# Kernel optimization log

Hardware: AMD Instinct MI355X
Metric: run time of the kernel (lower is better)

Reference implementation:

```python
import jax, jax.numpy as jnp
import numpy as np
from jax import lax

T, B, I, H = 512, 32, 1024, 1024


def setup_inputs() -> dict:
    key = jax.random.key(0)
    ks = jax.random.split(key, 9)
    s = 1.0 / np.sqrt(H)
    u = lambda k, shape: jax.random.uniform(k, shape, jnp.float32, -s, s)
    return {
        "x": jax.random.normal(ks[0], (T, B, I), jnp.float32),
        "h0_fwd": jnp.zeros((B, H), jnp.float32),
        "c0_fwd": jnp.zeros((B, H), jnp.float32),
        "h0_bwd": jnp.zeros((B, H), jnp.float32),
        "c0_bwd": jnp.zeros((B, H), jnp.float32),
        "Wih_f": u(ks[1], (4 * H, I)), "Whh_f": u(ks[2], (4 * H, H)),
        "bih_f": u(ks[3], (4 * H,)), "bhh_f": u(ks[4], (4 * H,)),
        "Wih_b": u(ks[5], (4 * H, I)), "Whh_b": u(ks[6], (4 * H, H)),
        "bih_b": u(ks[7], (4 * H,)), "bhh_b": u(ks[8], (4 * H,)),
    }


def _lstm_dir(x, h0, c0, Wih, Whh, bih, bhh, reverse):
    # Precompute input-to-gate projections for all timesteps: [T, B, 4H]
    xg = jnp.einsum('tbi,gi->tbg', x, Wih) + bih + bhh
    WhhT = Whh.T  # [H, 4H]

    def step(carry, xg_t):
        h, c = carry
        gates = xg_t + h @ WhhT  # [B, 4H]
        i, f, g, o = jnp.split(gates, 4, axis=-1)
        i = jax.nn.sigmoid(i)
        f = jax.nn.sigmoid(f)
        g = jnp.tanh(g)
        o = jax.nn.sigmoid(o)
        c = f * c + i * g
        h = o * jnp.tanh(c)
        return (h, c), h

    (hT, cT), ys = lax.scan(step, (h0, c0), xg, reverse=reverse)
    return ys, hT, cT


def reference(x, h0_fwd, c0_fwd, h0_bwd, c0_bwd,
              Wih_f, Whh_f, bih_f, bhh_f,
              Wih_b, Whh_b, bih_b, bhh_b):
    out_f, hf, cf = _lstm_dir(x, h0_fwd, c0_fwd, Wih_f, Whh_f, bih_f, bhh_f, reverse=False)
    out_b, hb, cb = _lstm_dir(x, h0_bwd, c0_bwd, Wih_b, Whh_b, bih_b, bhh_b, reverse=True)
    out = jnp.concatenate([out_f, out_b], axis=-1)  # [T, B, 2H]
    return out, (hf, cf), (hb, cb)
```

## Files before the change

kernel.cpp:

```cpp
#include <hip/hip_runtime.h>
#include <stdint.h>


using short8 = __attribute__((ext_vector_type(8))) short;
using f32x4  = __attribute__((ext_vector_type(4))) float;
using f32x2  = __attribute__((ext_vector_type(2))) float;
using f32x16 = __attribute__((ext_vector_type(16))) float;
using h2f    = __attribute__((ext_vector_type(2))) _Float16;

typedef unsigned int uint;
typedef unsigned short ushort;
typedef unsigned long long ull;

typedef const __attribute__((address_space(1))) void cg_void;
typedef __attribute__((address_space(3))) void lds_void;

#define OFF_XB      0ull
#define OFF_WIH_F   33554432ull
#define OFF_WIH_B   41943040ull
#define OFF_WHH_F   50331648ull
#define OFF_WHH_B   58720256ull
#define OFF_BSUM_F  67108864ull
#define OFF_BSUM_B  67125248ull
#define OFF_HBUF    67141632ull
#define OFF_CBUF    67665920ull
#define OFF_XG      67928064ull


__device__ __forceinline__ ushort f2bf(float f) {
    uint u = __float_as_uint(f);
    u += 0x7fffu + ((u >> 16) & 1u);
    return (ushort)(u >> 16);
}
__device__ __forceinline__ float sigmoidf_(float x) { return 1.0f / (1.0f + expf(-x)); }

__global__ __launch_bounds__(256) void prep_kernel(
    const float* __restrict__ x,
    const float* __restrict__ wih_f, const float* __restrict__ whh_f,
    const float* __restrict__ bih_f, const float* __restrict__ bhh_f,
    const float* __restrict__ wih_b, const float* __restrict__ whh_b,
    const float* __restrict__ bih_b, const float* __restrict__ bhh_b,
    const float* __restrict__ h0f, const float* __restrict__ h0b,
    char* __restrict__ ws)
{
    int r = blockIdx.x * 256 + threadIdx.x;
    const int n_x = 16777216, n_w = 4194304;
    if (r < n_x) { ((ushort*)(ws + OFF_XB))[r] = f2bf(x[r]); return; }
    r -= n_x;
    if (r < n_w) { ((ushort*)(ws + OFF_WIH_F))[r] = f2bf(wih_f[r]); return; }
    r -= n_w;
    if (r < n_w) { ((ushort*)(ws + OFF_WIH_B))[r] = f2bf(wih_b[r]); return; }
    r -= n_w;
    if (r < n_w) { ((ushort*)(ws + OFF_WHH_F))[r] = f2bf(whh_f[r]); return; }
    r -= n_w;
    if (r < n_w) { ((ushort*)(ws + OFF_WHH_B))[r] = f2bf(whh_b[r]); return; }
    r -= n_w;
    if (r < 4096) { ((float*)(ws + OFF_BSUM_F))[r] = bih_f[r] + bhh_f[r]; return; }
    r -= 4096;
    if (r < 4096) { ((float*)(ws + OFF_BSUM_B))[r] = bih_b[r] + bhh_b[r]; return; }
    r -= 4096;
    if (r < 16384) {
        int b = r >> 9, wi = r & 511;
        uint pay = (uint)f2bf(h0f[b * 1024 + wi * 2]) |
                   ((uint)f2bf(h0f[b * 1024 + wi * 2 + 1]) << 16);
        ((ull*)(ws + OFF_HBUF))[r] = (ull)pay;
        return;
    }
    r -= 16384;
    if (r < 16384) {
        int b = r >> 9, wi = r & 511;
        uint pay = (uint)f2bf(h0b[b * 1024 + wi * 2]) |
                   ((uint)f2bf(h0b[b * 1024 + wi * 2 + 1]) << 16);
        ((ull*)(ws + OFF_HBUF))[2 * 16384 + r] = (ull)pay;
        return;
    }
    r -= 16384;
    if (r < 32768) {
        size_t wd = (r < 16384) ? (size_t)(16384 + r) : (size_t)(3 * 16384 + (r - 16384));
        ((ull*)(ws + OFF_HBUF))[wd] = 0xFFFFFFFF00000000ull;
        return;
    }
}

__global__ __launch_bounds__(256) void gemm_xg(
    const ushort* __restrict__ xb,
    const ushort* __restrict__ wihf, const ushort* __restrict__ wihb,
    _Float16* __restrict__ xgf, _Float16* __restrict__ xgb,
    int s0)
{
    __shared__ ushort As[128 * 32];
    __shared__ ushort Bs[128 * 32];
    const int dir = blockIdx.z;
    const ushort* __restrict__ W = dir ? wihb : wihf;
    _Float16* __restrict__ xg = dir ? xgb : xgf;
    const int mBlk = blockIdx.x, nBlk = blockIdx.y;
    const int tid = threadIdx.x;
    const int w = tid >> 6, l = tid & 63;
    const int q = l >> 4, ml = l & 15;

    f32x4 acc[4][4];
    const f32x4 zero = {0.f, 0.f, 0.f, 0.f};
#pragma unroll
    for (int i = 0; i < 4; ++i)
#pragma unroll
        for (int j = 0; j < 4; ++j) acc[i][j] = zero;

    for (int kb = 0; kb < 32; ++kb) {
#pragma unroll
        for (int it = 0; it < 2; ++it) {
            int idx = tid + 256 * it;
            int rl = idx >> 2, kc = idx & 3;
            int gr = mBlk * 128 + rl;
            int slot = gr >> 5, bb = gr & 31;
            int t = dir ? (511 - s0 - slot) : (s0 + slot);
            const ushort* ga = xb + (size_t)(t * 32 + bb) * 1024 + kb * 32 + kc * 8;
            __builtin_amdgcn_global_load_lds((cg_void*)ga, (lds_void*)(As + idx * 8), 16, 0, 0);
            int colg = nBlk * 128 + rl;
            const ushort* gbp = W + (size_t)colg * 1024 + kb * 32 + kc * 8;
            __builtin_amdgcn_global_load_lds((cg_void*)gbp, (lds_void*)(Bs + idx * 8), 16, 0, 0);
        }
        __syncthreads();
        short8 af[4], bfr[4];
#pragma unroll
        for (int i = 0; i < 4; ++i)
            af[i] = *(const short8*)(As + ((w & 1) * 64 + i * 16 + ml) * 32 + q * 8);
#pragma unroll
        for (int j = 0; j < 4; ++j)
            bfr[j] = *(const short8*)(Bs + ((w >> 1) * 64 + j * 16 + ml) * 32 + q * 8);
#pragma unroll
        for (int i = 0; i < 4; ++i)
#pragma unroll
            for (int j = 0; j < 4; ++j)
                acc[i][j] = __builtin_amdgcn_mfma_f32_16x16x32_bf16(af[i], bfr[j], acc[i][j], 0, 0, 0);
        __syncthreads();
    }
#pragma unroll
    for (int i = 0; i < 4; ++i)
#pragma unroll
        for (int j = 0; j < 4; ++j)
#pragma unroll
            for (int rr = 0; rr < 4; ++rr) {
                int row = mBlk * 128 + (w & 1) * 64 + i * 16 + q * 4 + rr;
                int col = nBlk * 128 + (w >> 1) * 64 + j * 16 + ml;
                xg[(size_t)row * 4096 + col] = (_Float16)acc[i][j][rr];
            }
}

__global__ __launch_bounds__(512, 1) void rec_kernel(
    const ushort* __restrict__ whhf, const ushort* __restrict__ whhb,
    const _Float16* __restrict__ xgf, const _Float16* __restrict__ xgb,
    const float* __restrict__ bsumf, const float* __restrict__ bsumb,
    const float* __restrict__ c0f, const float* __restrict__ c0b,
    ull* __restrict__ hbuf, float* __restrict__ cbuf,
    float* __restrict__ out,
    int s0, int csteps)
{
    __shared__ __align__(16) char lds_raw[65536];
    ushort* Hst = (ushort*)lds_raw;
    float*  gb  = (float*)lds_raw;

    const int bx = blockIdx.x;
    const int dir = bx & 1;
    const int p = bx >> 1;
    const int tid = threadIdx.x;
    const int w = tid >> 6;
    const int l = tid & 63;
    const int half = l >> 5;
    const int m32 = l & 31;
    const int nt = w & 3;
    const int kh = w >> 2;

    const ushort* W = dir ? whhb : whhf;
    const _Float16* xg = dir ? xgb : xgf;
    const float* bsum = dir ? bsumb : bsumf;

    const ushort* wrow = W + ((size_t)(nt * 1024 + p * 32 + m32)) * 1024 + kh * 512 + half * 8;
    short8 bfrag[32];
#pragma unroll
    for (int kk = 0; kk < 32; ++kk)
        bfrag[kk] = *(const short8*)(wrow + kk * 16);

    const int b = tid >> 4;
    const int rp = (tid & 15) * 2;
    const int hcol = p * 32 + rp;
    f32x2 bs[4];
#pragma unroll
    for (int g = 0; g < 4; ++g)
        bs[g] = *(const f32x2*)(bsum + g * 1024 + hcol);
    f32x2 cc;
    {
        const float* csrc = (s0 == 0) ? (dir ? c0b : c0f) : (cbuf + dir * 32768);
        cc = *(const f32x2*)(csrc + b * 1024 + hcol);
    }

    const int ch = tid >> 2;
    const int sub = (tid & 3) * 2;

    for (int s = s0; s < s0 + csteps; ++s) {
        const int slot = s - s0;
        const int t = dir ? (511 - s) : s;

        uint xv[4];
#pragma unroll
        for (int g = 0; g < 4; ++g)
            xv[g] = *(const uint*)(xg + ((size_t)slot * 32 + b) * 4096 + g * 1024 + hcol);

        const ull* hb64 = hbuf + (size_t)(dir * 2 + (s & 1)) * 16384;
        const uint su = (uint)s;
        {
            ull cur[8], nxt[8];
#pragma unroll
            for (int j = 0; j < 8; ++j)
                cur[j] = __hip_atomic_load(hb64 + j * 512 + tid,
                                           __ATOMIC_RELAXED, __HIP_MEMORY_SCOPE_AGENT);
#pragma unroll
            for (int gI = 0; gI < 4; ++gI) {
                if (gI < 3) {
#pragma unroll
                    for (int j = 0; j < 8; ++j)
                        nxt[j] = __hip_atomic_load(hb64 + (gI * 8 + 8 + j) * 512 + tid,
                                                   __ATOMIC_RELAXED, __HIP_MEMORY_SCOPE_AGENT);
                }
                for (;;) {
                    bool bad = false;
#pragma unroll
                    for (int j = 0; j < 8; ++j)
                        bad = bad || ((uint)(cur[j] >> 32) != su);
                    if (!__any(bad)) break;
#pragma unroll
                    for (int j = 0; j < 8; ++j)
                        if ((uint)(cur[j] >> 32) != su)
                            cur[j] = __hip_atomic_load(hb64 + (gI * 8 + j) * 512 + tid,
                                                       __ATOMIC_RELAXED, __HIP_MEMORY_SCOPE_AGENT);
                }
#pragma unroll
                for (int j = 0; j < 8; ++j) {
                    const int bb = gI * 8 + j;
                    *(uint*)(Hst + bb * 1024 + ((ch ^ (bb & 7)) << 3) + sub) = (uint)cur[j];
                }
                if (gI < 3) {
#pragma unroll
                    for (int j = 0; j < 8; ++j) cur[j] = nxt[j];
                }
            }
        }
        __syncthreads();

        f32x16 acce, acco;
#pragma unroll
        for (int i = 0; i < 16; ++i) { acce[i] = 0.f; acco[i] = 0.f; }
#pragma unroll
        for (int kk = 0; kk < 32; kk += 2) {
            const short8 a0 = *(const short8*)(Hst + m32 * 1024 +
                (((kh * 64 + kk * 2 + half) ^ (m32 & 7)) << 3));
            acce = __builtin_amdgcn_mfma_f32_32x32x16_bf16(a0, bfrag[kk], acce, 0, 0, 0);
            const short8 a1 = *(const short8*)(Hst + m32 * 1024 +
                (((kh * 64 + (kk + 1) * 2 + half) ^ (m32 & 7)) << 3));
            acco = __builtin_amdgcn_mfma_f32_32x32x16_bf16(a1, bfrag[kk + 1], acco, 0, 0, 0);
        }
        __syncthreads();

#pragma unroll
        for (int reg = 0; reg < 16; ++reg) {
            const int row = (reg & 3) + 8 * (reg >> 2) + 4 * half;
            gb[kh * 4128 + row * 129 + nt * 32 + m32] = acce[reg] + acco[reg];
        }
        __syncthreads();

        const float* gA = gb + b * 129 + rp;
        const float* gB = gb + 4128 + b * 129 + rp;
        f32x2 G[4];
#pragma unroll
        for (int g = 0; g < 4; ++g) {
            h2f xh = __builtin_bit_cast(h2f, xv[g]);
            G[g][0] = gA[g * 32]     + gB[g * 32]     + bs[g][0] + (float)xh[0];
            G[g][1] = gA[g * 32 + 1] + gB[g * 32 + 1] + bs[g][1] + (float)xh[1];
        }
        f32x2 hh;
#pragma unroll
        for (int j = 0; j < 2; ++j) {
            float ii = sigmoidf_(G[0][j]), ff2 = sigmoidf_(G[1][j]);
            float g2 = tanhf(G[2][j]),     oo  = sigmoidf_(G[3][j]);
            cc[j] = ff2 * cc[j] + ii * g2;
            hh[j] = oo * tanhf(cc[j]);
        }
        {
            uint pay = (uint)f2bf(hh[0]) | ((uint)f2bf(hh[1]) << 16);
            ull word = (ull)pay | ((ull)(uint)(s + 1) << 32);
            __hip_atomic_store(hbuf + (size_t)(dir * 2 + ((s + 1) & 1)) * 16384 +
                                   b * 512 + p * 16 + (tid & 15),
                               word, __ATOMIC_RELAXED, __HIP_MEMORY_SCOPE_AGENT);
        }

        __builtin_nontemporal_store(__builtin_bit_cast(double, hh),
            (double*)(out + (size_t)t * 65536 + b * 2048 + dir * 1024 + hcol));
        if (s == 511) {
            float* fin = out + 33554432 + dir * 65536;
            *(f32x2*)(fin + b * 1024 + hcol) = hh;
            *(f32x2*)(fin + 32768 + b * 1024 + hcol) = cc;
        }
        __syncthreads();
    }
    *(f32x2*)(cbuf + dir * 32768 + b * 1024 + hcol) = cc;
}

extern "C" void kernel_launch(void* const* d_in, const int* in_sizes, int n_in,
                              void* d_out, int out_size, void* d_ws, size_t ws_size,
                              hipStream_t stream)
{
    const float* x     = (const float*)d_in[0];
    const float* h0f   = (const float*)d_in[1];
    const float* c0f   = (const float*)d_in[2];
    const float* h0b   = (const float*)d_in[3];
    const float* c0b   = (const float*)d_in[4];
    const float* wih_f = (const float*)d_in[5];
    const float* whh_f = (const float*)d_in[6];
    const float* bih_f = (const float*)d_in[7];
    const float* bhh_f = (const float*)d_in[8];
    const float* wih_b = (const float*)d_in[9];
    const float* whh_b = (const float*)d_in[10];
    const float* bih_b = (const float*)d_in[11];
    const float* bhh_b = (const float*)d_in[12];
    float* out = (float*)d_out;
    char* ws = (char*)d_ws;

    int csteps = 16;
    const int cands[6] = {512, 256, 128, 64, 32, 16};
    for (int i = 0; i < 6; ++i) {
        size_t need = OFF_XG + 2ull * (size_t)cands[i] * 262144ull;
        if (need <= ws_size) { csteps = cands[i]; break; }
    }

    prep_kernel<<<131360, 256, 0, stream>>>(x, wih_f, whh_f, bih_f, bhh_f,
                                            wih_b, whh_b, bih_b, bhh_b, h0f, h0b, ws);

    const ushort* xb    = (const ushort*)(ws + OFF_XB);
    const ushort* wihfb = (const ushort*)(ws + OFF_WIH_F);
    const ushort* wihbb = (const ushort*)(ws + OFF_WIH_B);
    const ushort* whhfb = (const ushort*)(ws + OFF_WHH_F);
    const ushort* whhbb = (const ushort*)(ws + OFF_WHH_B);
    const float*  bsf   = (const float*)(ws + OFF_BSUM_F);
    const float*  bsb   = (const float*)(ws + OFF_BSUM_B);
    ull*    hb          = (ull*)(ws + OFF_HBUF);
    float*  cb          = (float*)(ws + OFF_CBUF);
    _Float16* xgfp      = (_Float16*)(ws + OFF_XG);
    _Float16* xgbp      = (_Float16*)(ws + OFF_XG + (size_t)csteps * 262144ull);

    const int nchunks = 512 / csteps;
    for (int cidx = 0; cidx < nchunks; ++cidx) {
        int s0 = cidx * csteps;
        gemm_xg<<<dim3(csteps / 4, 32, 2), 256, 0, stream>>>(xb, wihfb, wihbb, xgfp, xgbp, s0);

        const ushort* a0 = whhfb; const ushort* a1 = whhbb;
        const _Float16* a2 = xgfp; const _Float16* a3 = xgbp;
        const float* a4 = bsf; const float* a5 = bsb;
        const float* a6 = c0f; const float* a7 = c0b;
        ull* a8 = hb; float* a9 = cb; float* a10 = out;
        int a11 = s0, a12 = csteps;
        void* args[] = {&a0, &a1, &a2, &a3, &a4, &a5, &a6, &a7, &a8, &a9, &a10, &a11, &a12};
        hipLaunchCooperativeKernel((void*)rec_kernel, dim3(64), dim3(512), args, 0, stream);
    }
}
```

Baseline: 3.598 ms.

## Fuse input-projection GEMM with recurrence using producer blocks and per-slab counters

Replaces the chunked sequence of GEMM plus cooperative recurrence launches with a single cooperative launch. In it, 192 blocks compute the input projection for all timesteps and publish per-4-step completion counters, while 64 recurrence blocks spin on those counters and consume the projections as they arrive. The GEMM is meant to overlap with the serial recurrence, and per-chunk launch and c-state spill overheads go away. The change also swaps expf and tanhf for exp2/rcp-based fast sigmoid and tanh, which reduces accuracy slightly. It assumes the workspace can hold the full projection buffer and relies on co-residency and spin-waits for correctness.

Result: faster. 3.001 ms (-16.6%).

```diff
diff --git a/kernel.cpp b/kernel.cpp
--- a/kernel.cpp
+++ b/kernel.cpp
@@ -23,16 +23,22 @@
 #define OFF_BSUM_F  67108864ull
 #define OFF_BSUM_B  67125248ull
 #define OFF_HBUF    67141632ull
-#define OFF_CBUF    67665920ull
-#define OFF_XG      67928064ull
-
+#define OFF_XGCNT   67665920ull
+#define OFF_XG      67667968ull
 
 __device__ __forceinline__ ushort f2bf(float f) {
     uint u = __float_as_uint(f);
     u += 0x7fffu + ((u >> 16) & 1u);
     return (ushort)(u >> 16);
 }
-__device__ __forceinline__ float sigmoidf_(float x) { return 1.0f / (1.0f + expf(-x)); }
+__device__ __forceinline__ float fsig(float x) {
+    float e = __builtin_amdgcn_exp2f(-1.4426950408889634f * x);
+    return __builtin_amdgcn_rcpf(1.0f + e);
+}
+__device__ __forceinline__ float ftanh(float x) {
+    float e = __builtin_amdgcn_exp2f(2.8853900817779268f * x);
+    return 1.0f - 2.0f * __builtin_amdgcn_rcpf(1.0f + e);
+}
 
 __global__ __launch_bounds__(256) void prep_kernel(
     const float* __restrict__ x,
@@ -80,91 +86,104 @@
         ((ull*)(ws + OFF_HBUF))[wd] = 0xFFFFFFFF00000000ull;
         return;
     }
-}
-
-__global__ __launch_bounds__(256) void gemm_xg(
+    r -= 32768;
+    if (r < 256) { ((uint*)(ws + OFF_XGCNT))[r] = 0u; return; }
+}
+
+__global__ __launch_bounds__(512, 1) void fused_kernel(
+    const ushort* __restrict__ whhf, const ushort* __restrict__ whhb,
     const ushort* __restrict__ xb,
     const ushort* __restrict__ wihf, const ushort* __restrict__ wihb,
     _Float16* __restrict__ xgf, _Float16* __restrict__ xgb,
-    int s0)
-{
-    __shared__ ushort As[128 * 32];
-    __shared__ ushort Bs[128 * 32];
-    const int dir = blockIdx.z;
-    const ushort* __restrict__ W = dir ? wihb : wihf;
-    _Float16* __restrict__ xg = dir ? xgb : xgf;
-    const int mBlk = blockIdx.x, nBlk = blockIdx.y;
-    const int tid = threadIdx.x;
-    const int w = tid >> 6, l = tid & 63;
-    const int q = l >> 4, ml = l & 15;
-
-    f32x4 acc[4][4];
-    const f32x4 zero = {0.f, 0.f, 0.f, 0.f};
-#pragma unroll
-    for (int i = 0; i < 4; ++i)
-#pragma unroll
-        for (int j = 0; j < 4; ++j) acc[i][j] = zero;
-
-    for (int kb = 0; kb < 32; ++kb) {
-#pragma unroll
-        for (int it = 0; it < 2; ++it) {
-            int idx = tid + 256 * it;
-            int rl = idx >> 2, kc = idx & 3;
-            int gr = mBlk * 128 + rl;
-            int slot = gr >> 5, bb = gr & 31;
-            int t = dir ? (511 - s0 - slot) : (s0 + slot);
-            const ushort* ga = xb + (size_t)(t * 32 + bb) * 1024 + kb * 32 + kc * 8;
-            __builtin_amdgcn_global_load_lds((cg_void*)ga, (lds_void*)(As + idx * 8), 16, 0, 0);
-            int colg = nBlk * 128 + rl;
-            const ushort* gbp = W + (size_t)colg * 1024 + kb * 32 + kc * 8;
-            __builtin_amdgcn_global_load_lds((cg_void*)gbp, (lds_void*)(Bs + idx * 8), 16, 0, 0);
-        }
-        __syncthreads();
-        short8 af[4], bfr[4];
-#pragma unroll
-        for (int i = 0; i < 4; ++i)
-            af[i] = *(const short8*)(As + ((w & 1) * 64 + i * 16 + ml) * 32 + q * 8);
-#pragma unroll
-        for (int j = 0; j < 4; ++j)
-            bfr[j] = *(const short8*)(Bs + ((w >> 1) * 64 + j * 16 + ml) * 32 + q * 8);
-#pragma unroll
-        for (int i = 0; i < 4; ++i)
-#pragma unroll
-            for (int j = 0; j < 4; ++j)
-                acc[i][j] = __builtin_amdgcn_mfma_f32_16x16x32_bf16(af[i], bfr[j], acc[i][j], 0, 0, 0);
-        __syncthreads();
-    }
-#pragma unroll
-    for (int i = 0; i < 4; ++i)
-#pragma unroll
-        for (int j = 0; j < 4; ++j)
-#pragma unroll
-            for (int rr = 0; rr < 4; ++rr) {
-                int row = mBlk * 128 + (w & 1) * 64 + i * 16 + q * 4 + rr;
-                int col = nBlk * 128 + (w >> 1) * 64 + j * 16 + ml;
-                xg[(size_t)row * 4096 + col] = (_Float16)acc[i][j][rr];
-            }
-}
-
-__global__ __launch_bounds__(512, 1) void rec_kernel(
-    const ushort* __restrict__ whhf, const ushort* __restrict__ whhb,
-    const _Float16* __restrict__ xgf, const _Float16* __restrict__ xgb,
     const float* __restrict__ bsumf, const float* __restrict__ bsumb,
     const float* __restrict__ c0f, const float* __restrict__ c0b,
-    ull* __restrict__ hbuf, float* __restrict__ cbuf,
-    float* __restrict__ out,
-    int s0, int csteps)
+    ull* __restrict__ hbuf, float* __restrict__ out,
+    uint* __restrict__ xgcnt)
 {
     __shared__ __align__(16) char lds_raw[65536];
+    const int tid = threadIdx.x;
+    const int w = tid >> 6;
+    const int l = tid & 63;
+
+    if (blockIdx.x >= 64) {
+        const int g = blockIdx.x - 64;
+        ushort* As = (ushort*)lds_raw;
+        ushort* Bs = (ushort*)lds_raw + 4096;
+        const int q = l >> 4, ml = l & 15;
+
+        for (int tau = g; tau < 4096; tau += 192) {
+            const int mg = tau >> 5, dir = (tau >> 4) & 1, n = tau & 15;
+            const ushort* Wn = (dir ? wihb : wihf) + (size_t)(n * 256) * 1024;
+            _Float16* xgd = dir ? xgb : xgf;
+
+            f32x4 acc[4][4];
+            const f32x4 zero = {0.f, 0.f, 0.f, 0.f};
+#pragma unroll
+            for (int i = 0; i < 4; ++i)
+#pragma unroll
+                for (int j = 0; j < 4; ++j) acc[i][j] = zero;
+
+            for (int kb = 0; kb < 32; ++kb) {
+                {
+                    int rl = tid >> 2, kc = tid & 3;
+                    int slot = mg * 4 + (rl >> 5), bb = rl & 31;
+                    int t = dir ? (511 - slot) : slot;
+                    const ushort* ga = xb + (size_t)(t * 32 + bb) * 1024 + kb * 32 + kc * 8;
+                    __builtin_amdgcn_global_load_lds((cg_void*)ga, (lds_void*)(As + tid * 8), 16, 0, 0);
+                }
+#pragma unroll
+                for (int it = 0; it < 2; ++it) {
+                    int idx = tid + 512 * it;
+                    int rl = idx >> 2, kc = idx & 3;
+                    const ushort* gbp = Wn + (size_t)rl * 1024 + kb * 32 + kc * 8;
+                    __builtin_amdgcn_global_load_lds((cg_void*)gbp, (lds_void*)(Bs + idx * 8), 16, 0, 0);
+                }
+                __syncthreads();
+                short8 af[4], bfr[4];
+#pragma unroll
+                for (int i = 0; i < 4; ++i)
+                    af[i] = *(const short8*)(As + ((w & 1) * 64 + i * 16 + ml) * 32 + q * 8);
+#pragma unroll
+                for (int j = 0; j < 4; ++j)
+                    bfr[j] = *(const short8*)(Bs + ((w >> 1) * 64 + j * 16 + ml) * 32 + q * 8);
+#pragma unroll
+                for (int i = 0; i < 4; ++i)
+#pragma unroll
+                    for (int j = 0; j < 4; ++j)
+                        acc[i][j] = __builtin_amdgcn_mfma_f32_16x16x32_bf16(af[i], bfr[j], acc[i][j], 0, 0, 0);
+                __syncthreads();
+            }
+            ushort* xgu = (ushort*)xgd;
+#pragma unroll
+            for (int i = 0; i < 4; ++i)
+#pragma unroll
+                for (int j = 0; j < 4; ++j)
+#pragma unroll
+                    for (int rr = 0; rr < 4; ++rr) {
+                        int trow = (w & 1) * 64 + i * 16 + q * 4 + rr;
+                        int col = n * 256 + (w >> 1) * 64 + j * 16 + ml;
+                        size_t grow = (size_t)(mg * 128 + trow);
+                        _Float16 v = (_Float16)acc[i][j][rr];
+                        __hip_atomic_store(xgu + grow * 4096 + col,
+                                           __builtin_bit_cast(ushort, v),
+                                           __ATOMIC_RELAXED, __HIP_MEMORY_SCOPE_AGENT);
+                    }
+            asm volatile("s_waitcnt vmcnt(0)" ::: "memory");
+            __syncthreads();
+            if (tid == 0)
+                __hip_atomic_fetch_add(xgcnt + dir * 128 + mg, 1u,
+                                       __ATOMIC_RELAXED, __HIP_MEMORY_SCOPE_AGENT);
+        }
+        return;
+    }
+
+    __builtin_amdgcn_s_setprio(1);
     ushort* Hst = (ushort*)lds_raw;
     float*  gb  = (float*)lds_raw;
 
     const int bx = blockIdx.x;
     const int dir = bx & 1;
     const int p = bx >> 1;
-    const int tid = threadIdx.x;
-    const int w = tid >> 6;
-    const int l = tid & 63;
     const int half = l >> 5;
     const int m32 = l & 31;
     const int nt = w & 3;
@@ -173,6 +192,7 @@
     const ushort* W = dir ? whhb : whhf;
     const _Float16* xg = dir ? xgb : xgf;
     const float* bsum = dir ? bsumb : bsumf;
+    const uint* xcnt = xgcnt + dir * 128;
 
     const ushort* wrow = W + ((size_t)(nt * 1024 + p * 32 + m32)) * 1024 + kh * 512 + half * 8;
     short8 bfrag[32];
@@ -185,25 +205,35 @@
     const int hcol = p * 32 + rp;
     f32x2 bs[4];
 #pragma unroll
-    for (int g = 0; g < 4; ++g)
-        bs[g] = *(const f32x2*)(bsum + g * 1024 + hcol);
+    for (int g2 = 0; g2 < 4; ++g2)
+        bs[g2] = *(const f32x2*)(bsum + g2 * 1024 + hcol);
     f32x2 cc;
     {
-        const float* csrc = (s0 == 0) ? (dir ? c0b : c0f) : (cbuf + dir * 32768);
+        const float* csrc = dir ? c0b : c0f;
         cc = *(const f32x2*)(csrc + b * 1024 + hcol);
     }
 
     const int ch = tid >> 2;
     const int sub = (tid & 3) * 2;
 
-    for (int s = s0; s < s0 + csteps; ++s) {
-        const int slot = s - s0;
+    for (int s = 0; s < 512; ++s) {
         const int t = dir ? (511 - s) : s;
 
+        if ((s & 3) == 0) {
+            const uint* cp = xcnt + (s >> 2);
+            uint c = __hip_atomic_load(cp, __ATOMIC_RELAXED, __HIP_MEMORY_SCOPE_AGENT);
+            while (c < 16u) {
+                __builtin_amdgcn_s_sleep(8);
+                c = __hip_atomic_load(cp, __ATOMIC_RELAXED, __HIP_MEMORY_SCOPE_AGENT);
+            }
+        }
+
         uint xv[4];
 #pragma unroll
-        for (int g = 0; g < 4; ++g)
-            xv[g] = *(const uint*)(xg + ((size_t)slot * 32 + b) * 4096 + g * 1024 + hcol);
+        for (int g2 = 0; g2 < 4; ++g2)
+            xv[g2] = __hip_atomic_load(
+                (const uint*)(xg + ((size_t)s * 32 + b) * 4096 + g2 * 1024 + hcol),
+                __ATOMIC_RELAXED, __HIP_MEMORY_SCOPE_AGENT);
 
         const ull* hb64 = hbuf + (size_t)(dir * 2 + (s & 1)) * 16384;
         const uint su = (uint)s;
@@ -271,18 +301,18 @@
         const float* gB = gb + 4128 + b * 129 + rp;
         f32x2 G[4];
 #pragma unroll
-        for (int g = 0; g < 4; ++g) {
-            h2f xh = __builtin_bit_cast(h2f, xv[g]);
-            G[g][0] = gA[g * 32]     + gB[g * 32]     + bs[g][0] + (float)xh[0];
-            G[g][1] = gA[g * 32 + 1] + gB[g * 32 + 1] + bs[g][1] + (float)xh[1];
+        for (int g2 = 0; g2 < 4; ++g2) {
+            h2f xh = __builtin_bit_cast(h2f, xv[g2]);
+            G[g2][0] = gA[g2 * 32]     + gB[g2 * 32]     + bs[g2][0] + (float)xh[0];
+            G[g2][1] = gA[g2 * 32 + 1] + gB[g2 * 32 + 1] + bs[g2][1] + (float)xh[1];
         }
         f32x2 hh;
 #pragma unroll
         for (int j = 0; j < 2; ++j) {
-            float ii = sigmoidf_(G[0][j]), ff2 = sigmoidf_(G[1][j]);
-            float g2 = tanhf(G[2][j]),     oo  = sigmoidf_(G[3][j]);
-            cc[j] = ff2 * cc[j] + ii * g2;
-            hh[j] = oo * tanhf(cc[j]);
+            float ii = fsig(G[0][j]), ff2 = fsig(G[1][j]);
+            float g2v = ftanh(G[2][j]), oo = fsig(G[3][j]);
+            cc[j] = ff2 * cc[j] + ii * g2v;
+            hh[j] = oo * ftanh(cc[j]);
         }
         {
             uint pay = (uint)f2bf(hh[0]) | ((uint)f2bf(hh[1]) << 16);
@@ -301,7 +331,6 @@
         }
         __syncthreads();
     }
-    *(f32x2*)(cbuf + dir * 32768 + b * 1024 + hcol) = cc;
 }
 
 extern "C" void kernel_launch(void* const* d_in, const int* in_sizes, int n_in,
@@ -324,17 +353,10 @@
     float* out = (float*)d_out;
     char* ws = (char*)d_ws;
 
-    int csteps = 16;
-    const int cands[6] = {512, 256, 128, 64, 32, 16};
-    for (int i = 0; i < 6; ++i) {
-        size_t need = OFF_XG + 2ull * (size_t)cands[i] * 262144ull;
-        if (need <= ws_size) { csteps = cands[i]; break; }
-    }
-
-    prep_kernel<<<131360, 256, 0, stream>>>(x, wih_f, whh_f, bih_f, bhh_f,
+    prep_kernel<<<131361, 256, 0, stream>>>(x, wih_f, whh_f, bih_f, bhh_f,
                                             wih_b, whh_b, bih_b, bhh_b, h0f, h0b, ws);
 
-    const ushort* xb    = (const ushort*)(ws + OFF_XB);
+    const ushort* xbp   = (const ushort*)(ws + OFF_XB);
     const ushort* wihfb = (const ushort*)(ws + OFF_WIH_F);
     const ushort* wihbb = (const ushort*)(ws + OFF_WIH_B);
     const ushort* whhfb = (const ushort*)(ws + OFF_WHH_F);
@@ -342,22 +364,18 @@
     const float*  bsf   = (const float*)(ws + OFF_BSUM_F);
     const float*  bsb   = (const float*)(ws + OFF_BSUM_B);
     ull*    hb          = (ull*)(ws + OFF_HBUF);
-    float*  cb          = (float*)(ws + OFF_CBUF);
+    uint*   xgcntp      = (uint*)(ws + OFF_XGCNT);
     _Float16* xgfp      = (_Float16*)(ws + OFF_XG);
-    _Float16* xgbp      = (_Float16*)(ws + OFF_XG + (size_t)csteps * 262144ull);
-
-    const int nchunks = 512 / csteps;
-    for (int cidx = 0; cidx < nchunks; ++cidx) {
-        int s0 = cidx * csteps;
-        gemm_xg<<<dim3(csteps / 4, 32, 2), 256, 0, stream>>>(xb, wihfb, wihbb, xgfp, xgbp, s0);
-
-        const ushort* a0 = whhfb; const ushort* a1 = whhbb;
-        const _Float16* a2 = xgfp; const _Float16* a3 = xgbp;
-        const float* a4 = bsf; const float* a5 = bsb;
-        const float* a6 = c0f; const float* a7 = c0b;
-        ull* a8 = hb; float* a9 = cb; float* a10 = out;
-        int a11 = s0, a12 = csteps;
-        void* args[] = {&a0, &a1, &a2, &a3, &a4, &a5, &a6, &a7, &a8, &a9, &a10, &a11, &a12};
-        hipLaunchCooperativeKernel((void*)rec_kernel, dim3(64), dim3(512), args, 0, stream);
-    }
-}
+    _Float16* xgbp      = (_Float16*)(ws + OFF_XG + 134217728ull);
+
+    const ushort* a0 = whhfb; const ushort* a1 = whhbb;
+    const ushort* a2 = xbp;
+    const ushort* a3 = wihfb; const ushort* a4 = wihbb;
+    _Float16* a5 = xgfp; _Float16* a6 = xgbp;
+    const float* a7 = bsf; const float* a8 = bsb;
+    const float* a9 = c0f; const float* a10 = c0b;
+    ull* a11 = hb; float* a12 = out; uint* a13 = xgcntp;
+    void* args[] = {&a0, &a1, &a2, &a3, &a4, &a5, &a6, &a7, &a8, &a9, &a10,
+                    &a11, &a12, &a13};
+    hipLaunchCooperativeKernel((void*)fused_kernel, dim3(256), dim3(512), args, 0, stream);
+}
```
